# Kernel optimization log

Measured on AMD Instinct MI355X. Metric: run time of the kernel, lower is better.

## Reference

```python
import jax, jax.numpy as jnp
import numpy as np

T = 1.0  # temperature (init kwarg t)
N, M, D = 16384, 16384, 64


def setup_inputs() -> dict:
    key = jax.random.key(0)
    k1, k2, k3 = jax.random.split(key, 3)
    logits = jax.random.normal(k1, (N, D), dtype=jnp.float32)
    targets = jax.random.normal(k2, (M, D), dtype=jnp.float32)
    # probabilities in (0,1]; bounded away from 0 so log is finite
    noise_probs = jax.random.uniform(k3, (D,), dtype=jnp.float32, minval=1e-3, maxval=1.0)
    return {"logits": logits, "targets": targets, "noise_probs": noise_probs}


def reference(logits, targets, noise_probs):
    # q: (N, d) = logits / t - log(noise_probs)
    q = logits / T - jnp.log(noise_probs)[None, :]
    # The torch repeat/unsqueeze/reshape broadcast-multiply-sum is exactly a GEMM:
    # scores[n, m] = sum_d q[n, d] * targets[m, d]
    scores = jnp.einsum('nd,md->nm', q, targets)  # (N, M)
    # subtract detached row max (numerical stabilization, no grad through max)
    scores = scores - jax.lax.stop_gradient(jnp.max(scores, axis=1, keepdims=True))
    # CrossEntropyLoss with labels = arange(N) (non-distributed path), mean reduction
    logp = jax.nn.log_softmax(scores, axis=1)  # (N, M)
    labels = jnp.arange(scores.shape[0])
    picked = jnp.take_along_axis(logp, labels[:, None], axis=1)[:, 0]  # (N,)
    return -jnp.mean(picked)
```

## Files before the change

### kernel.cpp

```cpp
#include <hip/hip_runtime.h>
#include <stdint.h>

#define N_ROWS 16384
#define NSPLIT 16
#define COLS_PER_SPLIT (N_ROWS / NSPLIT)
#define N_ITER (COLS_PER_SPLIT / 64)
#define SHIFT2 64.0f
#define LOG2E 1.44269504088896340736f
#define LN2 0.69314718055994530942f
#define POISON_U32 0xAAAAAAAAu

using short8  = __attribute__((ext_vector_type(8))) short;
using float4v = __attribute__((ext_vector_type(4))) float;

__device__ __forceinline__ unsigned short f2bf(float f) {
  unsigned u = __float_as_uint(f);
  unsigned r = (u + 0x7fffu + ((u >> 16) & 1u)) >> 16;
  return (unsigned short)r;
}
__device__ __forceinline__ float bf2f(unsigned short s) {
  return __uint_as_float(((unsigned)s) << 16);
}

__device__ __forceinline__ void async_stage_16(const void* g, void* l) {
  __builtin_amdgcn_global_load_lds(
      (const __attribute__((address_space(1))) uint32_t*)g,
      (__attribute__((address_space(3))) uint32_t*)l, 16, 0, 0);
}

__device__ __forceinline__ void stage_tile64(const uint8_t* gbase, uint8_t* lds,
                                             int wave, int lane) {
#pragma unroll
  for (int q = 0; q < 2; ++q) {
    int t = wave * 2 + q;
    int row = t * 8 + (lane >> 3);
    int c = (lane & 7) ^ (row & 7);
    async_stage_16(gbase + row * 128 + c * 16, lds + t * 1024 + lane * 16);
  }
}

__global__ void prep_kernel(const float4* __restrict__ lg,
                            const float4* __restrict__ tg,
                            const float* __restrict__ noise,
                            ushort4* __restrict__ qa,
                            ushort4* __restrict__ tb,
                            float* __restrict__ diag) {
  int tid = threadIdx.x;
  int i = blockIdx.x * blockDim.x + tid;
  int d4 = (i & 15) << 2;
  float4 l = lg[i];
  float4 t = tg[i];
  ushort4 ua, ub;
  ua.x = f2bf(l.x * LOG2E - log2f(noise[d4 + 0]));
  ua.y = f2bf(l.y * LOG2E - log2f(noise[d4 + 1]));
  ua.z = f2bf(l.z * LOG2E - log2f(noise[d4 + 2]));
  ua.w = f2bf(l.w * LOG2E - log2f(noise[d4 + 3]));
  ub.x = f2bf(t.x);
  ub.y = f2bf(t.y);
  ub.z = f2bf(t.z);
  ub.w = f2bf(t.w);
  qa[i] = ua;
  tb[i] = ub;

  float part = bf2f(ua.x) * bf2f(ub.x) + bf2f(ua.y) * bf2f(ub.y) +
               bf2f(ua.z) * bf2f(ub.z) + bf2f(ua.w) * bf2f(ub.w);
  part += __shfl_xor(part, 1);
  part += __shfl_xor(part, 2);
  part += __shfl_xor(part, 4);
  part += __shfl_xor(part, 8);
  if ((tid & 15) == 0) diag[i >> 4] = part;
}

__global__ __launch_bounds__(256, 4) void flash_kernel(
    const uint8_t* __restrict__ qa,
    const uint8_t* __restrict__ tb,
    const float* __restrict__ diag,
    float* __restrict__ row_sums,
    unsigned* __restrict__ cnt,
    unsigned* __restrict__ done_cnt,
    float* __restrict__ ws_loss,
    float* __restrict__ out) {
  __shared__ __align__(16) uint8_t ldsB0[64 * 128];
  __shared__ __align__(16) uint8_t ldsB1[64 * 128];
  __shared__ int is_last;

  const int bid = blockIdx.x;
  const int rb = bid >> 4;
  const int sp = bid & 15;
  const int tid = threadIdx.x;
  const int wave = tid >> 6;
  const int lane = tid & 63;
  const int m = lane & 15;
  const int kc = lane >> 4;

  const int row0 = rb * 128;
  const int col0 = sp * COLS_PER_SPLIT;
  const int rows_off = wave * 32;

  stage_tile64(tb + (size_t)col0 * 128, ldsB0, wave, lane);

  short8 afrag[2][2];
#pragma unroll
  for (int i = 0; i < 2; ++i)
#pragma unroll
    for (int k2 = 0; k2 < 2; ++k2)
      afrag[i][k2] = *(const short8*)(qa +
          (size_t)(row0 + rows_off + i * 16 + m) * 128 + (k2 * 4 + kc) * 16);

  float sums[2][4];
#pragma unroll
  for (int i = 0; i < 2; ++i)
#pragma unroll
    for (int r = 0; r < 4; ++r) sums[i][r] = 0.f;

  __syncthreads();

  auto do_tile = [&](const uint8_t* buf) {
    short8 bfrag[4][2];
#pragma unroll
    for (int j = 0; j < 4; ++j)
#pragma unroll
      for (int k2 = 0; k2 < 2; ++k2) {
        int r = j * 16 + m;
        int c = (k2 * 4 + kc) ^ (r & 7);
        bfrag[j][k2] = *(const short8*)(buf + r * 128 + c * 16);
      }
#pragma unroll
    for (int j = 0; j < 4; ++j) {
      float4v acc[2];
#pragma unroll
      for (int i = 0; i < 2; ++i) {
        float4v a0 = {-SHIFT2, -SHIFT2, -SHIFT2, -SHIFT2};
        a0 = __builtin_amdgcn_mfma_f32_16x16x32_bf16(afrag[i][0], bfrag[j][0], a0, 0, 0, 0);
        a0 = __builtin_amdgcn_mfma_f32_16x16x32_bf16(afrag[i][1], bfrag[j][1], a0, 0, 0, 0);
        acc[i] = a0;
      }
#pragma unroll
      for (int i = 0; i < 2; ++i)
#pragma unroll
        for (int r = 0; r < 4; ++r)
          sums[i][r] += __builtin_amdgcn_exp2f(acc[i][r]);
    }
  };

  for (int it2 = 0; it2 < N_ITER / 2; ++it2) {
    int t0 = it2 * 2;
    stage_tile64(tb + (size_t)(col0 + (t0 + 1) * 64) * 128, ldsB1, wave, lane);
    do_tile(ldsB0);
    __syncthreads();
    if (t0 + 2 < N_ITER)
      stage_tile64(tb + (size_t)(col0 + (t0 + 2) * 64) * 128, ldsB0, wave, lane);
    do_tile(ldsB1);
    __syncthreads();
  }

#pragma unroll
  for (int i = 0; i < 2; ++i)
#pragma unroll
    for (int r = 0; r < 4; ++r) {
      float v = sums[i][r];
      v += __shfl_xor(v, 1);
      v += __shfl_xor(v, 2);
      v += __shfl_xor(v, 4);
      v += __shfl_xor(v, 8);
      if (m == 0) {
        int grow = row0 + rows_off + i * 16 + kc * 4 + r;
        atomicAdd(&row_sums[grow], v);
      }
    }

  __syncthreads();
  if (tid == 0) {
    unsigned old = atomicAdd(&cnt[rb], 1u);
    is_last = (old == POISON_U32 + (NSPLIT - 1)) ? 1 : 0;
  }
  __syncthreads();

  if (is_last) {
    float part = 0.f;
    if (tid < 128) {
      int n = row0 + tid;
      float s = atomicAdd(&row_sums[n], 0.0f);
      part = LN2 * (SHIFT2 + log2f(s) - diag[n]);
    }
    part += __shfl_xor(part, 1);
    part += __shfl_xor(part, 2);
    part += __shfl_xor(part, 4);
    part += __shfl_xor(part, 8);
    part += __shfl_xor(part, 16);
    part += __shfl_xor(part, 32);
    if (tid < 128 && lane == 0) atomicAdd(ws_loss, part);
    __syncthreads();
    if (tid == 0) {
      unsigned old2 = atomicAdd(done_cnt, 1u);
      if (old2 == POISON_U32 + 127u) {
        float tot = atomicAdd(ws_loss, 0.0f);
        out[0] = tot * (1.0f / N_ROWS);
      }
    }
  }
}

extern "C" void kernel_launch(void* const* d_in, const int* in_sizes, int n_in,
                              void* d_out, int out_size, void* d_ws, size_t ws_size,
                              hipStream_t stream) {
  const float* logits  = (const float*)d_in[0];
  const float* targets = (const float*)d_in[1];
  const float* noise   = (const float*)d_in[2];
  float* out = (float*)d_out;

  uint8_t* ws = (uint8_t*)d_ws;
  uint8_t* qa = ws;
  uint8_t* tb = ws + (size_t)2 * 1024 * 1024;
  float* diag         = (float*)(ws + (size_t)4 * 1024 * 1024);
  float* row_sums     = (float*)(ws + (size_t)4 * 1024 * 1024 + 65536);
  unsigned* cnt       = (unsigned*)(ws + (size_t)4 * 1024 * 1024 + 131072);
  unsigned* done_cnt  = (unsigned*)(ws + (size_t)4 * 1024 * 1024 + 131072 + 512);
  float* ws_loss      = (float*)(ws + (size_t)4 * 1024 * 1024 + 131072 + 516);

  prep_kernel<<<1024, 256, 0, stream>>>(
      (const float4*)logits, (const float4*)targets, noise,
      (ushort4*)qa, (ushort4*)tb, diag);

  flash_kernel<<<128 * NSPLIT, 256, 0, stream>>>(
      qa, tb, diag, row_sums, cnt, done_cnt, ws_loss, out);
}
```

Baseline: 106.9 us.

## Load B fragments directly from global into registers instead of LDS staging

Drops the LDS double-buffered async staging of the target tile along with its block-wide barriers. Each wave now loads its B fragments straight from global memory into registers, double-buffered in registers. This removes the LDS traffic and __syncthreads, but every one of the four waves now fetches the same B tile separately, so global/L2 load traffic rises fourfold. It also raises register pressure under the 4-blocks-per-SM launch bound.

```diff
diff --git a/kernel.cpp b/kernel.cpp
--- a/kernel.cpp
+++ b/kernel.cpp
@@ -20,23 +20,6 @@
 }
 __device__ __forceinline__ float bf2f(unsigned short s) {
   return __uint_as_float(((unsigned)s) << 16);
-}
-
-__device__ __forceinline__ void async_stage_16(const void* g, void* l) {
-  __builtin_amdgcn_global_load_lds(
-      (const __attribute__((address_space(1))) uint32_t*)g,
-      (__attribute__((address_space(3))) uint32_t*)l, 16, 0, 0);
-}
-
-__device__ __forceinline__ void stage_tile64(const uint8_t* gbase, uint8_t* lds,
-                                             int wave, int lane) {
-#pragma unroll
-  for (int q = 0; q < 2; ++q) {
-    int t = wave * 2 + q;
-    int row = t * 8 + (lane >> 3);
-    int c = (lane & 7) ^ (row & 7);
-    async_stage_16(gbase + row * 128 + c * 16, lds + t * 1024 + lane * 16);
-  }
 }
 
 __global__ void prep_kernel(const float4* __restrict__ lg,
@@ -80,8 +63,6 @@
     unsigned* __restrict__ done_cnt,
     float* __restrict__ ws_loss,
     float* __restrict__ out) {
-  __shared__ __align__(16) uint8_t ldsB0[64 * 128];
-  __shared__ __align__(16) uint8_t ldsB1[64 * 128];
   __shared__ int is_last;
 
   const int bid = blockIdx.x;
@@ -97,8 +78,6 @@
   const int col0 = sp * COLS_PER_SPLIT;
   const int rows_off = wave * 32;
 
-  stage_tile64(tb + (size_t)col0 * 128, ldsB0, wave, lane);
-
   short8 afrag[2][2];
 #pragma unroll
   for (int i = 0; i < 2; ++i)
@@ -113,26 +92,27 @@
 #pragma unroll
     for (int r = 0; r < 4; ++r) sums[i][r] = 0.f;
 
-  __syncthreads();
-
-  auto do_tile = [&](const uint8_t* buf) {
-    short8 bfrag[4][2];
+  const uint8_t* bbase = tb + (size_t)(col0 + m) * 128 + kc * 16;
+
+  short8 bufA[4][2], bufB[4][2];
+
+  auto loadB = [&](short8 (&bf)[4][2], int t) {
 #pragma unroll
     for (int j = 0; j < 4; ++j)
 #pragma unroll
-      for (int k2 = 0; k2 < 2; ++k2) {
-        int r = j * 16 + m;
-        int c = (k2 * 4 + kc) ^ (r & 7);
-        bfrag[j][k2] = *(const short8*)(buf + r * 128 + c * 16);
-      }
+      for (int k2 = 0; k2 < 2; ++k2)
+        bf[j][k2] = *(const short8*)(bbase + (size_t)(t * 64 + j * 16) * 128 + k2 * 64);
+  };
+
+  auto comp = [&](short8 (&bf)[4][2]) {
 #pragma unroll
     for (int j = 0; j < 4; ++j) {
       float4v acc[2];
 #pragma unroll
       for (int i = 0; i < 2; ++i) {
         float4v a0 = {-SHIFT2, -SHIFT2, -SHIFT2, -SHIFT2};
-        a0 = __builtin_amdgcn_mfma_f32_16x16x32_bf16(afrag[i][0], bfrag[j][0], a0, 0, 0, 0);
-        a0 = __builtin_amdgcn_mfma_f32_16x16x32_bf16(afrag[i][1], bfrag[j][1], a0, 0, 0, 0);
+        a0 = __builtin_amdgcn_mfma_f32_16x16x32_bf16(afrag[i][0], bf[j][0], a0, 0, 0, 0);
+        a0 = __builtin_amdgcn_mfma_f32_16x16x32_bf16(afrag[i][1], bf[j][1], a0, 0, 0, 0);
         acc[i] = a0;
       }
 #pragma unroll
@@ -143,15 +123,12 @@
     }
   };
 
-  for (int it2 = 0; it2 < N_ITER / 2; ++it2) {
-    int t0 = it2 * 2;
-    stage_tile64(tb + (size_t)(col0 + (t0 + 1) * 64) * 128, ldsB1, wave, lane);
-    do_tile(ldsB0);
-    __syncthreads();
-    if (t0 + 2 < N_ITER)
-      stage_tile64(tb + (size_t)(col0 + (t0 + 2) * 64) * 128, ldsB0, wave, lane);
-    do_tile(ldsB1);
-    __syncthreads();
+  loadB(bufA, 0);
+  for (int t2 = 0; t2 < N_ITER / 2; ++t2) {
+    loadB(bufB, 2 * t2 + 1);
+    comp(bufA);
+    if (t2 < N_ITER / 2 - 1) loadB(bufA, 2 * t2 + 2);
+    comp(bufB);
   }
 
 #pragma unroll
```

Result: slower. 183.9 us (+72.0%).
